# Performance work log

Measured on AMD Instinct MI355X. Metric: run time of the kernel, lower is better.

Reference implementation:

```python
import jax, jax.numpy as jnp
import numpy as np
from jax import lax

N_FFT = 2048
HOP = 512
N_ITER = 60
MOMENTUM = 0.99 / (1.0 + 0.99)  # torchaudio normalizes momentum/(1+momentum)
EPS = 1e-16
PAD = N_FFT // 2


def _hann(n):
    # periodic hann window, matches torch.hann_window(n)
    return 0.5 - 0.5 * jnp.cos(2.0 * jnp.pi * jnp.arange(n, dtype=jnp.float32) / n)


def _stft(x, window):
    # x: (B, L) real -> (B, F, T) complex. center=True, reflect pad, onesided, unnormalized.
    B, L = x.shape
    xp = jnp.pad(x, ((0, 0), (PAD, PAD)), mode='reflect')
    T = 1 + (L + 2 * PAD - N_FFT) // HOP
    idx = jnp.arange(T)[:, None] * HOP + jnp.arange(N_FFT)[None, :]  # (T, N)
    frames = xp[:, idx] * window  # (B, T, N)
    spec = jnp.fft.rfft(frames, axis=-1)  # (B, T, F)
    return jnp.swapaxes(spec, 1, 2)  # (B, F, T)


def _istft(spec, window):
    # spec: (B, F, T) complex -> (B, hop*(T-1)) real. Matches torch.istft(center=True).
    B, F, T = spec.shape
    frames = jnp.fft.irfft(jnp.swapaxes(spec, 1, 2), n=N_FFT, axis=-1) * window  # (B, T, N)
    L_pad = N_FFT + HOP * (T - 1)
    idx_flat = (jnp.arange(T)[:, None] * HOP + jnp.arange(N_FFT)[None, :]).reshape(-1)
    y = jnp.zeros((B, L_pad), frames.dtype).at[:, idx_flat].add(frames.reshape(B, -1))
    wsq = jnp.zeros((L_pad,), window.dtype).at[idx_flat].add(
        jnp.tile(window * window, T))
    y = y / jnp.where(wsq > 1e-11, wsq, 1.0)
    return y[:, PAD:L_pad - PAD]


def _griffin_lim(spec, window):
    # spec: (B, F, T) nonnegative magnitudes (power=1.0 so no pow needed)
    spec_c = spec.astype(jnp.complex64)
    angles0 = jnp.ones_like(spec_c)   # rand_init=False -> full of ones
    tprev0 = jnp.zeros_like(spec_c)

    def step(carry, _):
        angles, tprev = carry
        inv = _istft(spec_c * angles, window)
        rebuilt = _stft(inv, window)
        a = rebuilt - tprev * MOMENTUM
        a = a / (jnp.abs(a) + EPS)
        return (a, rebuilt), None

    (angles, _), _ = lax.scan(step, (angles0, tprev0), None, length=N_ITER)
    return _istft(spec_c * angles, window)


def setup_inputs() -> dict:
    key = jax.random.key(0)
    B, T, F = 4, 400, N_FFT // 2 + 1
    spectrogram = jax.random.uniform(key, (B, T, F), dtype=jnp.float32)
    return {"spectrogram": spectrogram}


def reference(spectrogram):
    window = _hann(N_FFT)
    spec = jnp.transpose(spectrogram, (0, 2, 1))  # (B, F, T)
    return _griffin_lim(spec, window)  # (B, HOP*(T-1))
```

## Files before the change

kernel.cpp:

```cpp
#include <hip/hip_runtime.h>
#include <math.h>

constexpr int BB   = 4;
constexpr int TT   = 400;
constexpr int FF   = 1025;
constexpr int NFFT = 2048;
constexpr int HOP  = 512;
constexpr int PADD = 1024;
constexpr int LL   = HOP * (TT - 1);
constexpr int LPAD = NFFT + HOP * (TT - 1);
constexpr int NITER = 60;
constexpr double MOM = 0.99 / 1.99;
constexpr double EPSV = 1e-16;
constexpr double DPI = 3.14159265358979323846;

constexpr size_t OFF_TW1024 = 0;
constexpr size_t OFF_TW2048 = 2048;
constexpr size_t OFF_TPR    = 4098;
constexpr size_t OFF_FRM    = 3284098;
constexpr size_t OFF_XP     = 6560898;
constexpr size_t OFF_WIN32  = 7386242;
constexpr size_t OFF_WSQ32  = 7387266;
constexpr size_t WS_DOUBLES = 7490434;

__device__ __forceinline__ double2 cmuld(double2 a, double2 b) {
    return make_double2(a.x * b.x - a.y * b.y, a.x * b.y + a.y * b.x);
}

__device__ __forceinline__ int swz(int f) { return f ^ ((f >> 4) & 7); }

__device__ __forceinline__ float np_cosf(float x) {
    const float rint_cvt = 0x1.800000p+23f;
    float qf = __builtin_fmaf(x, 0x1.45f306p-1f, rint_cvt) - rint_cvt;
    float r = __builtin_fmaf(qf, -0x1.921fb0p+0f, x);
    r = __builtin_fmaf(qf, -0x1.5110b4p-22f, r);
    r = __builtin_fmaf(qf, -0x1.846988p-48f, r);
    r = __builtin_fmaf(qf, -0x1.8cc966p-73f, r);
    int q = (int)qf + 1;
    float r2 = r * r;
    float cosp = __builtin_fmaf(0x1.98e616p-16f, r2, -0x1.6c06dcp-10f);
    cosp = __builtin_fmaf(cosp, r2, 0x1.55553cp-5f);
    cosp = __builtin_fmaf(cosp, r2, -0x1.000000p-1f);
    cosp = __builtin_fmaf(cosp, r2, 0x1.000000p+0f);
    float sinp = __builtin_fmaf(0x1.7d3bbcp-19f, r2, -0x1.a06bbap-13f);
    sinp = __builtin_fmaf(sinp, r2, 0x1.11119ap-7f);
    sinp = __builtin_fmaf(sinp, r2, -0x1.555548p-3f);
    sinp = sinp * r2;
    sinp = __builtin_fmaf(sinp, r, r);
    float res = (q & 1) ? cosp : sinp;
    return (q & 2) ? -res : res;
}

__global__ void k_init_tables(double2* tw1024, double2* tw2048, float* win) {
    int n = blockIdx.x * blockDim.x + threadIdx.x;
    if (n < 1024) {
        double th = -2.0 * DPI * (double)n / 1024.0;
        double s, c; sincos(th, &s, &c);
        tw1024[n] = make_double2(c, s);
    }
    if (n < 1025) {
        double th = -2.0 * DPI * (double)n / 2048.0;
        double s, c; sincos(th, &s, &c);
        tw2048[n] = make_double2(c, s);
    }
    if (n < 2048) {
        const float TWO_PI_F = 6.283185307179586f;
        float ang = __fdiv_rn(__fmul_rn(TWO_PI_F, (float)n), 2048.0f);
        float c = np_cosf(ang);
        win[n] = __fsub_rn(0.5f, __fmul_rn(0.5f, c));
    }
}

__global__ void k_init_wsq(const float* __restrict__ win, float* __restrict__ wsq) {
    int m = blockIdx.x * blockDim.x + threadIdx.x;
    if (m >= LPAD) return;
    int tlo = (m - (NFFT - HOP)) >> 9;
    if (tlo < 0) tlo = 0;
    int thi = m >> 9;
    if (thi > TT - 1) thi = TT - 1;
    float s = 0.0f;
    for (int t = tlo; t <= thi; ++t) {
        float w = win[m - (t << 9)];
        s = __fadd_rn(s, __fmul_rn(w, w));
    }
    wsq[m] = (s > 1e-11f) ? s : 1.0f;
}

__global__ void k_init_state(double2* __restrict__ tpr) {
    int i = blockIdx.x * blockDim.x + threadIdx.x;
    if (i < BB * TT * FF) tpr[i] = make_double2(0.0, 0.0);
}

template <int DIR, bool TW>
__device__ __forceinline__ void bfly4(double2 a, double2 b, double2 c, double2 d,
                                      double2 w1, double2 w2, double2 w3,
                                      double2& o0, double2& o1, double2& o2, double2& o3) {
    if (TW) {
        if (DIR > 0) { w1.y = -w1.y; w2.y = -w2.y; w3.y = -w3.y; }
        b = cmuld(b, w1);
        c = cmuld(c, w2);
        d = cmuld(d, w3);
    }
    double2 u0 = make_double2(a.x + c.x, a.y + c.y);
    double2 u1 = make_double2(a.x - c.x, a.y - c.y);
    double2 v0 = make_double2(b.x + d.x, b.y + d.y);
    double2 v1 = make_double2(b.x - d.x, b.y - d.y);
    o0 = make_double2(u0.x + v0.x, u0.y + v0.y);
    o2 = make_double2(u0.x - v0.x, u0.y - v0.y);
    if (DIR < 0) {
        o1 = make_double2(u1.x + v1.y, u1.y - v1.x);
        o3 = make_double2(u1.x - v1.y, u1.y + v1.x);
    } else {
        o1 = make_double2(u1.x - v1.y, u1.y + v1.x);
        o3 = make_double2(u1.x + v1.y, u1.y - v1.x);
    }
}

template <int DIR>
__device__ void fft1024_reg(double2 r[16], double2* S, const double2* __restrict__ tw, int tid) {
    const double2 wid = make_double2(1.0, 0.0);
    double2 e[4][4];
#pragma unroll
    for (int m = 0; m < 4; ++m)
        bfly4<DIR, false>(r[m], r[m + 4], r[m + 8], r[m + 12], wid, wid, wid,
                          e[m][0], e[m][1], e[m][2], e[m][3]);
    double2 g[4][4];
#pragma unroll
    for (int r1 = 0; r1 < 4; ++r1) {
        int t1 = r1 << 6;
        bfly4<DIR, true>(e[0][r1], e[1][r1], e[2][r1], e[3][r1],
                         tw[t1 & 1023], tw[(2 * t1) & 1023], tw[(3 * t1) & 1023],
                         g[r1][0], g[r1][1], g[r1][2], g[r1][3]);
    }
#pragma unroll
    for (int r1 = 0; r1 < 4; ++r1)
#pragma unroll
        for (int u = 0; u < 4; ++u)
            S[swz(16 * tid + r1 + 4 * u)] = g[r1][u];
    __syncthreads();
    double2 r2[16];
#pragma unroll
    for (int j = 0; j < 16; ++j) r2[j] = S[swz(tid + 64 * j)];
    const int kapp = tid & 15;
    const int aa = tid >> 4;
    double2 h[4][4];
    {
        int t = kapp << 4;
        double2 w1 = tw[t & 1023], w2 = tw[(2 * t) & 1023], w3 = tw[(3 * t) & 1023];
#pragma unroll
        for (int m = 0; m < 4; ++m)
            bfly4<DIR, true>(r2[m], r2[m + 4], r2[m + 8], r2[m + 12], w1, w2, w3,
                             h[m][0], h[m][1], h[m][2], h[m][3]);
    }
    double2 gg[4][4];
#pragma unroll
    for (int u = 0; u < 4; ++u) {
        int t = (kapp + 16 * u) << 2;
        bfly4<DIR, true>(h[0][u], h[1][u], h[2][u], h[3][u],
                         tw[t & 1023], tw[(2 * t) & 1023], tw[(3 * t) & 1023],
                         gg[u][0], gg[u][1], gg[u][2], gg[u][3]);
    }
#pragma unroll
    for (int u = 0; u < 4; ++u)
#pragma unroll
        for (int w = 0; w < 4; ++w)
            S[swz(256 * aa + kapp + 16 * u + 64 * w)] = gg[u][w];
    __syncthreads();
    double2 r4[16];
#pragma unroll
    for (int j = 0; j < 16; ++j) r4[j] = S[swz(tid + 64 * j)];
#pragma unroll
    for (int m = 0; m < 4; ++m) {
        int t = tid + 64 * m;
        bfly4<DIR, true>(r4[m], r4[m + 4], r4[m + 8], r4[m + 12],
                         tw[t & 1023], tw[(2 * t) & 1023], tw[(3 * t) & 1023],
                         r[m], r[m + 4], r[m + 8], r[m + 12]);
    }
}

__device__ __forceinline__ double2 phase_step(double2 zk, double2 zc, double2 w,
                                              double2 tp, float mgf, double2* Xk_out) {
    zc.y = -zc.y;
    double2 A = make_double2(0.5 * (zk.x + zc.x), 0.5 * (zk.y + zc.y));
    double2 D = make_double2(zk.x - zc.x, zk.y - zc.y);
    double2 Bv = make_double2(0.5 * D.y, -0.5 * D.x);
    double2 wB = cmuld(w, Bv);
    double2 Xk = make_double2(A.x + wB.x, A.y + wB.y);
    double2 a = make_double2(Xk.x - MOM * tp.x, Xk.y - MOM * tp.y);
    double r = sqrt(a.x * a.x + a.y * a.y);
    double d = r + EPSV;
    *Xk_out = Xk;
    double m = (double)mgf;
    return make_double2(m * (a.x / d), m * (a.y / d));
}

__device__ __forceinline__ double2 pretwist(double2 Xk, double2 Xc, double2 w) {
    Xc.y = -Xc.y;
    double2 A = make_double2(0.5 * (Xk.x + Xc.x), 0.5 * (Xk.y + Xc.y));
    double2 D = make_double2(0.5 * (Xk.x - Xc.x), 0.5 * (Xk.y - Xc.y));
    w.y = -w.y;
    double2 Bv = cmuld(w, D);
    return make_double2(A.x - Bv.y, A.y + Bv.x);
}

template <int DIR>
__device__ void fft1024_w(double2* buf, const double2* __restrict__ tw, int tid) {
#pragma unroll
    for (int s = 0; s < 5; ++s) {
        const int p = 1 << (2 * s);
        double2 o0[4], o1[4], o2[4], o3[4];
        int jj[4];
#pragma unroll
        for (int q = 0; q < 4; ++q) {
            int v = tid + 64 * q;
            int k = v & (p - 1);
            jj[q] = ((v - k) << 2) + k;
            int t1 = k << (8 - 2 * s);
            bfly4<DIR, true>(buf[v], buf[v + 256], buf[v + 512], buf[v + 768],
                             tw[t1 & 1023], tw[(2 * t1) & 1023], tw[(3 * t1) & 1023],
                             o0[q], o1[q], o2[q], o3[q]);
        }
        __syncthreads();
#pragma unroll
        for (int q = 0; q < 4; ++q) {
            buf[jj[q]]         = o0[q];
            buf[jj[q] + p]     = o1[q];
            buf[jj[q] + 2 * p] = o2[q];
            buf[jj[q] + 3 * p] = o3[q];
        }
        __syncthreads();
    }
}

__global__ __launch_bounds__(64) void k_istft_first(
    const float* __restrict__ mag,
    const double2* __restrict__ tw1024, const double2* __restrict__ tw2048,
    const float* __restrict__ win, double* __restrict__ frames_out) {
    __shared__ double2 S[1025];
    const int fid = blockIdx.x;
    const int tid = threadIdx.x;
    const float* mg = mag + (size_t)fid * FF;
#pragma unroll
    for (int q = 0; q < 8; ++q) {
        int k = tid + 64 * q;
        double mk = (double)mg[k];
        if (k == 0) {
            double m1024 = (double)mg[1024];
            double m512  = (double)mg[512];
            S[0]   = pretwist(make_double2(mk, 0.0),   make_double2(m1024, 0.0), tw2048[0]);
            S[512] = pretwist(make_double2(m512, 0.0), make_double2(m512, 0.0),  tw2048[512]);
        } else {
            int kp = 1024 - k;
            double mp = (double)mg[kp];
            S[k]  = pretwist(make_double2(mk, 0.0), make_double2(mp, 0.0), tw2048[k]);
            S[kp] = pretwist(make_double2(mp, 0.0), make_double2(mk, 0.0), tw2048[kp]);
        }
    }
    __syncthreads();
    fft1024_w<1>(S, tw1024, tid);
    double2* fr = reinterpret_cast<double2*>(frames_out + (size_t)fid * NFFT);
    const float2* w2 = reinterpret_cast<const float2*>(win);
#pragma unroll
    for (int q = 0; q < 16; ++q) {
        int m = tid + 64 * q;
        double2 z = S[m];
        float2 wv = w2[m];
        fr[m] = make_double2(z.x * (1.0 / 1024.0) * (double)wv.x,
                             z.y * (1.0 / 1024.0) * (double)wv.y);
    }
}

__global__ __launch_bounds__(256) void k_ola(
    const double* __restrict__ frames, const float* __restrict__ wsq,
    double* __restrict__ xp) {
    int bx = blockIdx.x;
    int bid = (bx & 7) * 403 + (bx >> 3);
    int gid = bid * 256 + threadIdx.x;
    int b = gid / LPAD;
    int p = gid - b * LPAD;
    int j = p - PADD;
    if (j < 0) j = -j;
    else if (j >= LL) j = 2 * LL - 2 - j;
    int m = j + PADD;
    int tlo = (m - (NFFT - HOP)) >> 9;
    if (tlo < 0) tlo = 0;
    int thi = m >> 9;
    if (thi > TT - 1) thi = TT - 1;
    const double* fb = frames + (size_t)b * TT * NFFT;
    double s = 0.0;
    for (int t = tlo; t <= thi; ++t) s += fb[(size_t)t * NFFT + (m - (t << 9))];
    xp[gid] = s / (double)wsq[m];
}

__global__ __launch_bounds__(64) void k_fused(
    const double* __restrict__ xp, double* __restrict__ frames_out,
    const float* __restrict__ mag, double2* __restrict__ tpr,
    const double2* __restrict__ tw1024, const double2* __restrict__ tw2048,
    const float* __restrict__ win) {
    __shared__ double2 S[1024];
    const int bx = blockIdx.x;
    const int fid = (bx & 7) * 200 + (bx >> 3);
    const int b = fid / TT;
    const int t = fid - b * TT;
    const int tid = threadIdx.x;
    const double2* xb = reinterpret_cast<const double2*>(xp + (size_t)b * LPAD + (size_t)t * HOP);
    const float2* w2 = reinterpret_cast<const float2*>(win);
    double2 r[16];
#pragma unroll
    for (int j = 0; j < 16; ++j) {
        int k = tid + 64 * j;
        double2 v = xb[k];
        float2 wv = w2[k];
        r[j] = make_double2(v.x * (double)wv.x, v.y * (double)wv.y);
    }
    fft1024_reg<-1>(r, S, tw1024, tid);
#pragma unroll
    for (int j = 0; j < 16; ++j) S[swz(tid + 64 * j)] = r[j];
    __syncthreads();
    size_t base = (size_t)fid * FF;
    const float* mg = mag + base;
#pragma unroll
    for (int q = 0; q < 8; ++q) {
        int k = tid + 64 * q;
        int kp = 1024 - k;
        double2 zk = S[swz(k)];
        double2 zc = S[swz(kp & 1023)];
        double2 wk = tw2048[k];
        double2 Xk;
        double2 Snew_k = phase_step(zk, zc, wk, tpr[base + k], mg[k], &Xk);
        tpr[base + k] = Xk;
        if (k == 0) {
            double2 X1024;
            double2 Snew_1024 = phase_step(zk, zk, tw2048[1024], tpr[base + 1024], mg[1024], &X1024);
            tpr[base + 1024] = X1024;
            double2 z512 = S[swz(512)];
            double2 X512;
            double2 Snew_512 = phase_step(z512, z512, tw2048[512], tpr[base + 512], mg[512], &X512);
            tpr[base + 512] = X512;
            double2 Xk0 = Snew_k;    Xk0.y = 0.0;
            double2 Xc0 = Snew_1024; Xc0.y = 0.0;
            S[swz(0)]   = pretwist(Xk0, Xc0, tw2048[0]);
            S[swz(512)] = pretwist(Snew_512, Snew_512, tw2048[512]);
        } else {
            double2 wp = tw2048[kp];
            double2 Xp;
            double2 Snew_p = phase_step(zc, zk, wp, tpr[base + kp], mg[kp], &Xp);
            tpr[base + kp] = Xp;
            S[swz(k)]  = pretwist(Snew_k, Snew_p, wk);
            S[swz(kp)] = pretwist(Snew_p, Snew_k, wp);
        }
    }
    __syncthreads();
#pragma unroll
    for (int j = 0; j < 16; ++j) r[j] = S[swz(tid + 64 * j)];
    fft1024_reg<1>(r, S, tw1024, tid);
    double2* fr = reinterpret_cast<double2*>(frames_out + (size_t)fid * NFFT);
#pragma unroll
    for (int j = 0; j < 16; ++j) {
        int m = tid + 64 * j;
        float2 wv = w2[m];
        fr[m] = make_double2(r[j].x * (1.0 / 1024.0) * (double)wv.x,
                             r[j].y * (1.0 / 1024.0) * (double)wv.y);
    }
}

__global__ __launch_bounds__(256) void k_ola_out(
    const double* __restrict__ frames, const float* __restrict__ wsq,
    float* __restrict__ out) {
    int bx = blockIdx.x;
    int bid = (bx & 7) * 399 + (bx >> 3);
    int gid = bid * 256 + threadIdx.x;
    int b = gid / LL;
    int j = gid - b * LL;
    int m = j + PADD;
    int tlo = (m - (NFFT - HOP)) >> 9;
    if (tlo < 0) tlo = 0;
    int thi = m >> 9;
    if (thi > TT - 1) thi = TT - 1;
    const double* fb = frames + (size_t)b * TT * NFFT;
    double s = 0.0;
    for (int t = tlo; t <= thi; ++t) s += fb[(size_t)t * NFFT + (m - (t << 9))];
    out[gid] = (float)(s / (double)wsq[m]);
}

extern "C" void kernel_launch(void* const* d_in, const int* in_sizes, int n_in,
                              void* d_out, int out_size, void* d_ws, size_t ws_size,
                              hipStream_t stream) {
    if (ws_size < WS_DOUBLES * sizeof(double)) return;
    const float* mag = (const float*)d_in[0];
    double* ws = (double*)d_ws;
    double2* tw1024 = (double2*)(ws + OFF_TW1024);
    double2* tw2048 = (double2*)(ws + OFF_TW2048);
    double2* tprv   = (double2*)(ws + OFF_TPR);
    double* frames  = ws + OFF_FRM;
    double* xp      = ws + OFF_XP;
    float* win      = (float*)(ws + OFF_WIN32);
    float* wsq      = (float*)(ws + OFF_WSQ32);

    k_init_tables<<<8, 256, 0, stream>>>(tw1024, tw2048, win);
    k_init_wsq<<<LPAD / 256, 256, 0, stream>>>(win, wsq);
    k_init_state<<<(BB * TT * FF + 255) / 256, 256, 0, stream>>>(tprv);

    k_istft_first<<<BB * TT, 64, 0, stream>>>(mag, tw1024, tw2048, win, frames);
    for (int it = 0; it < NITER; ++it) {
        k_ola<<<(BB * LPAD) / 256, 256, 0, stream>>>(frames, wsq, xp);
        k_fused<<<BB * TT, 64, 0, stream>>>(xp, frames, mag, tprv,
                                            tw1024, tw2048, win);
    }
    k_ola_out<<<(BB * LL) / 256, 256, 0, stream>>>(frames, wsq, (float*)d_out);
}
```

Measured before the change: 1.776 ms.

## Fuse overlap-add into per-frame STFT kernel with ping-pong frame buffers

Removes the separate overlap-add kernel and its intermediate padded signal buffer by having each frame block gather and normalize its overlapping frame contributions directly before the forward FFT. Frames are double-buffered so reads and writes within one launch do not race. This halves the launches per iteration and removes a global write/read pass, at the cost of redundant gathers (each sample recomputed by up to four frames) done by low-occupancy 64-thread blocks.

```diff
diff --git a/kernel.cpp b/kernel.cpp
--- a/kernel.cpp
+++ b/kernel.cpp
@@ -17,11 +17,11 @@
 constexpr size_t OFF_TW1024 = 0;
 constexpr size_t OFF_TW2048 = 2048;
 constexpr size_t OFF_TPR    = 4098;
-constexpr size_t OFF_FRM    = 3284098;
-constexpr size_t OFF_XP     = 6560898;
-constexpr size_t OFF_WIN32  = 7386242;
-constexpr size_t OFF_WSQ32  = 7387266;
-constexpr size_t WS_DOUBLES = 7490434;
+constexpr size_t OFF_FRM0   = 3284098;
+constexpr size_t OFF_FRM1   = 6560898;
+constexpr size_t OFF_WIN32  = 9837698;
+constexpr size_t OFF_WSQ32  = 9838722;
+constexpr size_t WS_DOUBLES = 9941890;
 
 __device__ __forceinline__ double2 cmuld(double2 a, double2 b) {
     return make_double2(a.x * b.x - a.y * b.y, a.x * b.y + a.y * b.x);
@@ -270,48 +270,43 @@
     }
 }
 
-__global__ __launch_bounds__(256) void k_ola(
-    const double* __restrict__ frames, const float* __restrict__ wsq,
-    double* __restrict__ xp) {
-    int bx = blockIdx.x;
-    int bid = (bx & 7) * 403 + (bx >> 3);
-    int gid = bid * 256 + threadIdx.x;
-    int b = gid / LPAD;
-    int p = gid - b * LPAD;
-    int j = p - PADD;
-    if (j < 0) j = -j;
-    else if (j >= LL) j = 2 * LL - 2 - j;
-    int m = j + PADD;
-    int tlo = (m - (NFFT - HOP)) >> 9;
-    if (tlo < 0) tlo = 0;
-    int thi = m >> 9;
-    if (thi > TT - 1) thi = TT - 1;
-    const double* fb = frames + (size_t)b * TT * NFFT;
-    double s = 0.0;
-    for (int t = tlo; t <= thi; ++t) s += fb[(size_t)t * NFFT + (m - (t << 9))];
-    xp[gid] = s / (double)wsq[m];
-}
-
-__global__ __launch_bounds__(64) void k_fused(
-    const double* __restrict__ xp, double* __restrict__ frames_out,
+__global__ __launch_bounds__(64) void k_mono(
+    const double* __restrict__ frames_in, double* __restrict__ frames_out,
     const float* __restrict__ mag, double2* __restrict__ tpr,
     const double2* __restrict__ tw1024, const double2* __restrict__ tw2048,
-    const float* __restrict__ win) {
+    const float* __restrict__ win, const float* __restrict__ wsq) {
     __shared__ double2 S[1024];
     const int bx = blockIdx.x;
     const int fid = (bx & 7) * 200 + (bx >> 3);
     const int b = fid / TT;
     const int t = fid - b * TT;
     const int tid = threadIdx.x;
-    const double2* xb = reinterpret_cast<const double2*>(xp + (size_t)b * LPAD + (size_t)t * HOP);
     const float2* w2 = reinterpret_cast<const float2*>(win);
+    const double* fb = frames_in + (size_t)b * TT * NFFT;
+    const int t512 = t * HOP;
     double2 r[16];
 #pragma unroll
     for (int j = 0; j < 16; ++j) {
         int k = tid + 64 * j;
-        double2 v = xb[k];
+        double xv0, xv1;
+#pragma unroll
+        for (int h = 0; h < 2; ++h) {
+            int p = t512 + 2 * k + h;
+            int jj = p - PADD;
+            if (jj < 0) jj = -jj;
+            else if (jj >= LL) jj = 2 * LL - 2 - jj;
+            int m = jj + PADD;
+            int tlo = (m - (NFFT - HOP)) >> 9;
+            if (tlo < 0) tlo = 0;
+            int thi = m >> 9;
+            if (thi > TT - 1) thi = TT - 1;
+            double s = 0.0;
+            for (int u = tlo; u <= thi; ++u) s += fb[(size_t)u * NFFT + (m - (u << 9))];
+            double val = s / (double)wsq[m];
+            if (h == 0) xv0 = val; else xv1 = val;
+        }
         float2 wv = w2[k];
-        r[j] = make_double2(v.x * (double)wv.x, v.y * (double)wv.y);
+        r[j] = make_double2(xv0 * (double)wv.x, xv1 * (double)wv.y);
     }
     fft1024_reg<-1>(r, S, tw1024, tid);
 #pragma unroll
@@ -392,8 +387,8 @@
     double2* tw1024 = (double2*)(ws + OFF_TW1024);
     double2* tw2048 = (double2*)(ws + OFF_TW2048);
     double2* tprv   = (double2*)(ws + OFF_TPR);
-    double* frames  = ws + OFF_FRM;
-    double* xp      = ws + OFF_XP;
+    double* frm0    = ws + OFF_FRM0;
+    double* frm1    = ws + OFF_FRM1;
     float* win      = (float*)(ws + OFF_WIN32);
     float* wsq      = (float*)(ws + OFF_WSQ32);
 
@@ -401,11 +396,12 @@
     k_init_wsq<<<LPAD / 256, 256, 0, stream>>>(win, wsq);
     k_init_state<<<(BB * TT * FF + 255) / 256, 256, 0, stream>>>(tprv);
 
-    k_istft_first<<<BB * TT, 64, 0, stream>>>(mag, tw1024, tw2048, win, frames);
+    k_istft_first<<<BB * TT, 64, 0, stream>>>(mag, tw1024, tw2048, win, frm0);
     for (int it = 0; it < NITER; ++it) {
-        k_ola<<<(BB * LPAD) / 256, 256, 0, stream>>>(frames, wsq, xp);
-        k_fused<<<BB * TT, 64, 0, stream>>>(xp, frames, mag, tprv,
-                                            tw1024, tw2048, win);
-    }
-    k_ola_out<<<(BB * LL) / 256, 256, 0, stream>>>(frames, wsq, (float*)d_out);
-}
+        double* fin  = (it & 1) ? frm1 : frm0;
+        double* fout = (it & 1) ? frm0 : frm1;
+        k_mono<<<BB * TT, 64, 0, stream>>>(fin, fout, mag, tprv,
+                                           tw1024, tw2048, win, wsq);
+    }
+    k_ola_out<<<(BB * LL) / 256, 256, 0, stream>>>(frm0, wsq, (float*)d_out);
+}
```

Result: slower. 3.047 ms (+71.5%).

## Process two frames per block in fused STFT kernel to share barriers

Applied to the files above, without the earlier changes.

The fused per-iteration kernel now handles two frames per 64-thread block. The two 1024-point FFTs are interleaved stage by stage, so each shared-memory barrier and the twiddle loads are shared between them and there is more independent work per thread. Stores to shared memory are also issued right after each butterfly. The launch uses half as many blocks. In exchange, registers and LDS per block double (two 16 KB buffers), which can lower occupancy and leaves only 800 blocks to spread across the CUs.

```diff
diff --git a/kernel.cpp b/kernel.cpp
--- a/kernel.cpp
+++ b/kernel.cpp
@@ -117,30 +117,29 @@
 }
 
 template <int DIR>
-__device__ void fft1024_reg(double2 r[16], double2* S, const double2* __restrict__ tw, int tid) {
+__device__ __forceinline__ void fft_stage01(double2 r[16], double2* S, const double2* __restrict__ tw, int tid) {
     const double2 wid = make_double2(1.0, 0.0);
     double2 e[4][4];
 #pragma unroll
     for (int m = 0; m < 4; ++m)
         bfly4<DIR, false>(r[m], r[m + 4], r[m + 8], r[m + 12], wid, wid, wid,
                           e[m][0], e[m][1], e[m][2], e[m][3]);
-    double2 g[4][4];
 #pragma unroll
     for (int r1 = 0; r1 < 4; ++r1) {
+        double2 g0, g1, g2, g3;
         int t1 = r1 << 6;
         bfly4<DIR, true>(e[0][r1], e[1][r1], e[2][r1], e[3][r1],
                          tw[t1 & 1023], tw[(2 * t1) & 1023], tw[(3 * t1) & 1023],
-                         g[r1][0], g[r1][1], g[r1][2], g[r1][3]);
-    }
-#pragma unroll
-    for (int r1 = 0; r1 < 4; ++r1)
-#pragma unroll
-        for (int u = 0; u < 4; ++u)
-            S[swz(16 * tid + r1 + 4 * u)] = g[r1][u];
-    __syncthreads();
-    double2 r2[16];
-#pragma unroll
-    for (int j = 0; j < 16; ++j) r2[j] = S[swz(tid + 64 * j)];
+                         g0, g1, g2, g3);
+        S[swz(16 * tid + r1)]      = g0;
+        S[swz(16 * tid + r1 + 4)]  = g1;
+        S[swz(16 * tid + r1 + 8)]  = g2;
+        S[swz(16 * tid + r1 + 12)] = g3;
+    }
+}
+
+template <int DIR>
+__device__ __forceinline__ void fft_stage23(double2 r2[16], double2* S, const double2* __restrict__ tw, int tid) {
     const int kapp = tid & 15;
     const int aa = tid >> 4;
     double2 h[4][4];
@@ -152,23 +151,22 @@
             bfly4<DIR, true>(r2[m], r2[m + 4], r2[m + 8], r2[m + 12], w1, w2, w3,
                              h[m][0], h[m][1], h[m][2], h[m][3]);
     }
-    double2 gg[4][4];
 #pragma unroll
     for (int u = 0; u < 4; ++u) {
+        double2 g0, g1, g2, g3;
         int t = (kapp + 16 * u) << 2;
         bfly4<DIR, true>(h[0][u], h[1][u], h[2][u], h[3][u],
                          tw[t & 1023], tw[(2 * t) & 1023], tw[(3 * t) & 1023],
-                         gg[u][0], gg[u][1], gg[u][2], gg[u][3]);
-    }
-#pragma unroll
-    for (int u = 0; u < 4; ++u)
-#pragma unroll
-        for (int w = 0; w < 4; ++w)
-            S[swz(256 * aa + kapp + 16 * u + 64 * w)] = gg[u][w];
-    __syncthreads();
-    double2 r4[16];
-#pragma unroll
-    for (int j = 0; j < 16; ++j) r4[j] = S[swz(tid + 64 * j)];
+                         g0, g1, g2, g3);
+        S[swz(256 * aa + kapp + 16 * u)]       = g0;
+        S[swz(256 * aa + kapp + 16 * u + 64)]  = g1;
+        S[swz(256 * aa + kapp + 16 * u + 128)] = g2;
+        S[swz(256 * aa + kapp + 16 * u + 192)] = g3;
+    }
+}
+
+template <int DIR>
+__device__ __forceinline__ void fft_stage4(double2 r4[16], double2 r[16], const double2* __restrict__ tw, int tid) {
 #pragma unroll
     for (int m = 0; m < 4; ++m) {
         int t = tid + 64 * m;
@@ -176,6 +174,29 @@
                          tw[t & 1023], tw[(2 * t) & 1023], tw[(3 * t) & 1023],
                          r[m], r[m + 4], r[m + 8], r[m + 12]);
     }
+}
+
+template <int DIR>
+__device__ void fft1024_reg2(double2 rA[16], double2 rB[16], double2* SA, double2* SBl,
+                             const double2* __restrict__ tw, int tid) {
+    fft_stage01<DIR>(rA, SA, tw, tid);
+    fft_stage01<DIR>(rB, SBl, tw, tid);
+    __syncthreads();
+    double2 r2A[16], r2B[16];
+#pragma unroll
+    for (int j = 0; j < 16; ++j) r2A[j] = SA[swz(tid + 64 * j)];
+#pragma unroll
+    for (int j = 0; j < 16; ++j) r2B[j] = SBl[swz(tid + 64 * j)];
+    fft_stage23<DIR>(r2A, SA, tw, tid);
+    fft_stage23<DIR>(r2B, SBl, tw, tid);
+    __syncthreads();
+    double2 r4A[16], r4B[16];
+#pragma unroll
+    for (int j = 0; j < 16; ++j) r4A[j] = SA[swz(tid + 64 * j)];
+#pragma unroll
+    for (int j = 0; j < 16; ++j) r4B[j] = SBl[swz(tid + 64 * j)];
+    fft_stage4<DIR>(r4A, rA, tw, tid);
+    fft_stage4<DIR>(r4B, rB, tw, tid);
 }
 
 __device__ __forceinline__ double2 phase_step(double2 zk, double2 zc, double2 w,
@@ -203,122 +224,9 @@
     return make_double2(A.x - Bv.y, A.y + Bv.x);
 }
 
-template <int DIR>
-__device__ void fft1024_w(double2* buf, const double2* __restrict__ tw, int tid) {
-#pragma unroll
-    for (int s = 0; s < 5; ++s) {
-        const int p = 1 << (2 * s);
-        double2 o0[4], o1[4], o2[4], o3[4];
-        int jj[4];
-#pragma unroll
-        for (int q = 0; q < 4; ++q) {
-            int v = tid + 64 * q;
-            int k = v & (p - 1);
-            jj[q] = ((v - k) << 2) + k;
-            int t1 = k << (8 - 2 * s);
-            bfly4<DIR, true>(buf[v], buf[v + 256], buf[v + 512], buf[v + 768],
-                             tw[t1 & 1023], tw[(2 * t1) & 1023], tw[(3 * t1) & 1023],
-                             o0[q], o1[q], o2[q], o3[q]);
-        }
-        __syncthreads();
-#pragma unroll
-        for (int q = 0; q < 4; ++q) {
-            buf[jj[q]]         = o0[q];
-            buf[jj[q] + p]     = o1[q];
-            buf[jj[q] + 2 * p] = o2[q];
-            buf[jj[q] + 3 * p] = o3[q];
-        }
-        __syncthreads();
-    }
-}
-
-__global__ __launch_bounds__(64) void k_istft_first(
-    const float* __restrict__ mag,
-    const double2* __restrict__ tw1024, const double2* __restrict__ tw2048,
-    const float* __restrict__ win, double* __restrict__ frames_out) {
-    __shared__ double2 S[1025];
-    const int fid = blockIdx.x;
-    const int tid = threadIdx.x;
-    const float* mg = mag + (size_t)fid * FF;
-#pragma unroll
-    for (int q = 0; q < 8; ++q) {
-        int k = tid + 64 * q;
-        double mk = (double)mg[k];
-        if (k == 0) {
-            double m1024 = (double)mg[1024];
-            double m512  = (double)mg[512];
-            S[0]   = pretwist(make_double2(mk, 0.0),   make_double2(m1024, 0.0), tw2048[0]);
-            S[512] = pretwist(make_double2(m512, 0.0), make_double2(m512, 0.0),  tw2048[512]);
-        } else {
-            int kp = 1024 - k;
-            double mp = (double)mg[kp];
-            S[k]  = pretwist(make_double2(mk, 0.0), make_double2(mp, 0.0), tw2048[k]);
-            S[kp] = pretwist(make_double2(mp, 0.0), make_double2(mk, 0.0), tw2048[kp]);
-        }
-    }
-    __syncthreads();
-    fft1024_w<1>(S, tw1024, tid);
-    double2* fr = reinterpret_cast<double2*>(frames_out + (size_t)fid * NFFT);
-    const float2* w2 = reinterpret_cast<const float2*>(win);
-#pragma unroll
-    for (int q = 0; q < 16; ++q) {
-        int m = tid + 64 * q;
-        double2 z = S[m];
-        float2 wv = w2[m];
-        fr[m] = make_double2(z.x * (1.0 / 1024.0) * (double)wv.x,
-                             z.y * (1.0 / 1024.0) * (double)wv.y);
-    }
-}
-
-__global__ __launch_bounds__(256) void k_ola(
-    const double* __restrict__ frames, const float* __restrict__ wsq,
-    double* __restrict__ xp) {
-    int bx = blockIdx.x;
-    int bid = (bx & 7) * 403 + (bx >> 3);
-    int gid = bid * 256 + threadIdx.x;
-    int b = gid / LPAD;
-    int p = gid - b * LPAD;
-    int j = p - PADD;
-    if (j < 0) j = -j;
-    else if (j >= LL) j = 2 * LL - 2 - j;
-    int m = j + PADD;
-    int tlo = (m - (NFFT - HOP)) >> 9;
-    if (tlo < 0) tlo = 0;
-    int thi = m >> 9;
-    if (thi > TT - 1) thi = TT - 1;
-    const double* fb = frames + (size_t)b * TT * NFFT;
-    double s = 0.0;
-    for (int t = tlo; t <= thi; ++t) s += fb[(size_t)t * NFFT + (m - (t << 9))];
-    xp[gid] = s / (double)wsq[m];
-}
-
-__global__ __launch_bounds__(64) void k_fused(
-    const double* __restrict__ xp, double* __restrict__ frames_out,
-    const float* __restrict__ mag, double2* __restrict__ tpr,
-    const double2* __restrict__ tw1024, const double2* __restrict__ tw2048,
-    const float* __restrict__ win) {
-    __shared__ double2 S[1024];
-    const int bx = blockIdx.x;
-    const int fid = (bx & 7) * 200 + (bx >> 3);
-    const int b = fid / TT;
-    const int t = fid - b * TT;
-    const int tid = threadIdx.x;
-    const double2* xb = reinterpret_cast<const double2*>(xp + (size_t)b * LPAD + (size_t)t * HOP);
-    const float2* w2 = reinterpret_cast<const float2*>(win);
-    double2 r[16];
-#pragma unroll
-    for (int j = 0; j < 16; ++j) {
-        int k = tid + 64 * j;
-        double2 v = xb[k];
-        float2 wv = w2[k];
-        r[j] = make_double2(v.x * (double)wv.x, v.y * (double)wv.y);
-    }
-    fft1024_reg<-1>(r, S, tw1024, tid);
-#pragma unroll
-    for (int j = 0; j < 16; ++j) S[swz(tid + 64 * j)] = r[j];
-    __syncthreads();
-    size_t base = (size_t)fid * FF;
-    const float* mg = mag + base;
+__device__ __forceinline__ void middle_phase(double2* S, double2* __restrict__ tpr,
+                                             size_t base, const float* __restrict__ mg,
+                                             const double2* __restrict__ tw2048, int tid) {
 #pragma unroll
     for (int q = 0; q < 8; ++q) {
         int k = tid + 64 * q;
@@ -350,17 +258,148 @@
             S[swz(kp)] = pretwist(Snew_p, Snew_k, wp);
         }
     }
+}
+
+template <int DIR>
+__device__ void fft1024_w(double2* buf, const double2* __restrict__ tw, int tid) {
+#pragma unroll
+    for (int s = 0; s < 5; ++s) {
+        const int p = 1 << (2 * s);
+        double2 o0[4], o1[4], o2[4], o3[4];
+        int jj[4];
+#pragma unroll
+        for (int q = 0; q < 4; ++q) {
+            int v = tid + 64 * q;
+            int k = v & (p - 1);
+            jj[q] = ((v - k) << 2) + k;
+            int t1 = k << (8 - 2 * s);
+            bfly4<DIR, true>(buf[v], buf[v + 256], buf[v + 512], buf[v + 768],
+                             tw[t1 & 1023], tw[(2 * t1) & 1023], tw[(3 * t1) & 1023],
+                             o0[q], o1[q], o2[q], o3[q]);
+        }
+        __syncthreads();
+#pragma unroll
+        for (int q = 0; q < 4; ++q) {
+            buf[jj[q]]         = o0[q];
+            buf[jj[q] + p]     = o1[q];
+            buf[jj[q] + 2 * p] = o2[q];
+            buf[jj[q] + 3 * p] = o3[q];
+        }
+        __syncthreads();
+    }
+}
+
+__global__ __launch_bounds__(64) void k_istft_first(
+    const float* __restrict__ mag,
+    const double2* __restrict__ tw1024, const double2* __restrict__ tw2048,
+    const float* __restrict__ win, double* __restrict__ frames_out) {
+    __shared__ double2 S[1025];
+    const int fid = blockIdx.x;
+    const int tid = threadIdx.x;
+    const float* mg = mag + (size_t)fid * FF;
+#pragma unroll
+    for (int q = 0; q < 8; ++q) {
+        int k = tid + 64 * q;
+        double mk = (double)mg[k];
+        if (k == 0) {
+            double m1024 = (double)mg[1024];
+            double m512  = (double)mg[512];
+            S[0]   = pretwist(make_double2(mk, 0.0),   make_double2(m1024, 0.0), tw2048[0]);
+            S[512] = pretwist(make_double2(m512, 0.0), make_double2(m512, 0.0),  tw2048[512]);
+        } else {
+            int kp = 1024 - k;
+            double mp = (double)mg[kp];
+            S[k]  = pretwist(make_double2(mk, 0.0), make_double2(mp, 0.0), tw2048[k]);
+            S[kp] = pretwist(make_double2(mp, 0.0), make_double2(mk, 0.0), tw2048[kp]);
+        }
+    }
     __syncthreads();
-#pragma unroll
-    for (int j = 0; j < 16; ++j) r[j] = S[swz(tid + 64 * j)];
-    fft1024_reg<1>(r, S, tw1024, tid);
+    fft1024_w<1>(S, tw1024, tid);
     double2* fr = reinterpret_cast<double2*>(frames_out + (size_t)fid * NFFT);
+    const float2* w2 = reinterpret_cast<const float2*>(win);
+#pragma unroll
+    for (int q = 0; q < 16; ++q) {
+        int m = tid + 64 * q;
+        double2 z = S[m];
+        float2 wv = w2[m];
+        fr[m] = make_double2(z.x * (1.0 / 1024.0) * (double)wv.x,
+                             z.y * (1.0 / 1024.0) * (double)wv.y);
+    }
+}
+
+__global__ __launch_bounds__(256) void k_ola(
+    const double* __restrict__ frames, const float* __restrict__ wsq,
+    double* __restrict__ xp) {
+    int bx = blockIdx.x;
+    int bid = (bx & 7) * 403 + (bx >> 3);
+    int gid = bid * 256 + threadIdx.x;
+    int b = gid / LPAD;
+    int p = gid - b * LPAD;
+    int j = p - PADD;
+    if (j < 0) j = -j;
+    else if (j >= LL) j = 2 * LL - 2 - j;
+    int m = j + PADD;
+    int tlo = (m - (NFFT - HOP)) >> 9;
+    if (tlo < 0) tlo = 0;
+    int thi = m >> 9;
+    if (thi > TT - 1) thi = TT - 1;
+    const double* fb = frames + (size_t)b * TT * NFFT;
+    double s = 0.0;
+    for (int t = tlo; t <= thi; ++t) s += fb[(size_t)t * NFFT + (m - (t << 9))];
+    xp[gid] = s / (double)wsq[m];
+}
+
+__global__ __launch_bounds__(64) void k_fused(
+    const double* __restrict__ xp, double* __restrict__ frames_out,
+    const float* __restrict__ mag, double2* __restrict__ tpr,
+    const double2* __restrict__ tw1024, const double2* __restrict__ tw2048,
+    const float* __restrict__ win) {
+    __shared__ double2 SA[1024];
+    __shared__ double2 SBl[1024];
+    const int bx = blockIdx.x;
+    const int s = (bx & 7) * 100 + (bx >> 3);
+    const int fid0 = 2 * s;
+    const int fid1 = 2 * s + 1;
+    const int b0 = fid0 / TT, t0 = fid0 - b0 * TT;
+    const int b1 = fid1 / TT, t1 = fid1 - b1 * TT;
+    const int tid = threadIdx.x;
+    const double2* xb0 = reinterpret_cast<const double2*>(xp + (size_t)b0 * LPAD + (size_t)t0 * HOP);
+    const double2* xb1 = reinterpret_cast<const double2*>(xp + (size_t)b1 * LPAD + (size_t)t1 * HOP);
+    const float2* w2 = reinterpret_cast<const float2*>(win);
+    double2 rA[16], rB[16];
+#pragma unroll
+    for (int j = 0; j < 16; ++j) {
+        int k = tid + 64 * j;
+        float2 wv = w2[k];
+        double2 v0 = xb0[k];
+        double2 v1 = xb1[k];
+        rA[j] = make_double2(v0.x * (double)wv.x, v0.y * (double)wv.y);
+        rB[j] = make_double2(v1.x * (double)wv.x, v1.y * (double)wv.y);
+    }
+    fft1024_reg2<-1>(rA, rB, SA, SBl, tw1024, tid);
+#pragma unroll
+    for (int j = 0; j < 16; ++j) SA[swz(tid + 64 * j)] = rA[j];
+#pragma unroll
+    for (int j = 0; j < 16; ++j) SBl[swz(tid + 64 * j)] = rB[j];
+    __syncthreads();
+    middle_phase(SA,  tpr, (size_t)fid0 * FF, mag + (size_t)fid0 * FF, tw2048, tid);
+    middle_phase(SBl, tpr, (size_t)fid1 * FF, mag + (size_t)fid1 * FF, tw2048, tid);
+    __syncthreads();
+#pragma unroll
+    for (int j = 0; j < 16; ++j) rA[j] = SA[swz(tid + 64 * j)];
+#pragma unroll
+    for (int j = 0; j < 16; ++j) rB[j] = SBl[swz(tid + 64 * j)];
+    fft1024_reg2<1>(rA, rB, SA, SBl, tw1024, tid);
+    double2* fr0 = reinterpret_cast<double2*>(frames_out + (size_t)fid0 * NFFT);
+    double2* fr1 = reinterpret_cast<double2*>(frames_out + (size_t)fid1 * NFFT);
 #pragma unroll
     for (int j = 0; j < 16; ++j) {
         int m = tid + 64 * j;
         float2 wv = w2[m];
-        fr[m] = make_double2(r[j].x * (1.0 / 1024.0) * (double)wv.x,
-                             r[j].y * (1.0 / 1024.0) * (double)wv.y);
+        fr0[m] = make_double2(rA[j].x * (1.0 / 1024.0) * (double)wv.x,
+                              rA[j].y * (1.0 / 1024.0) * (double)wv.y);
+        fr1[m] = make_double2(rB[j].x * (1.0 / 1024.0) * (double)wv.x,
+                              rB[j].y * (1.0 / 1024.0) * (double)wv.y);
     }
 }
 
@@ -404,8 +443,8 @@
     k_istft_first<<<BB * TT, 64, 0, stream>>>(mag, tw1024, tw2048, win, frames);
     for (int it = 0; it < NITER; ++it) {
         k_ola<<<(BB * LPAD) / 256, 256, 0, stream>>>(frames, wsq, xp);
-        k_fused<<<BB * TT, 64, 0, stream>>>(xp, frames, mag, tprv,
-                                            tw1024, tw2048, win);
+        k_fused<<<BB * TT / 2, 64, 0, stream>>>(xp, frames, mag, tprv,
+                                                tw1024, tw2048, win);
     }
     k_ola_out<<<(BB * LL) / 256, 256, 0, stream>>>(frames, wsq, (float*)d_out);
 }
```

Measured after the change: 2.129 ms. +19.9%, slower.

## Recompute previous-iteration STFT instead of storing tprev state in global memory

Applied to the files above, without the earlier changes.

Removes the per-bin tprev buffer (read and write of complex doubles every iteration). Instead, the previous iteration's time-domain signal is kept in a ping-pong xp buffer and re-transformed with a second FFT inside the fused kernel to recover the previous rebuilt spectrum. This trades global-memory traffic for a doubled forward-FFT workload and twice the shared memory per block, which may reduce occupancy.

```diff
diff --git a/kernel.cpp b/kernel.cpp
--- a/kernel.cpp
+++ b/kernel.cpp
@@ -16,12 +16,12 @@
 
 constexpr size_t OFF_TW1024 = 0;
 constexpr size_t OFF_TW2048 = 2048;
-constexpr size_t OFF_TPR    = 4098;
-constexpr size_t OFF_FRM    = 3284098;
-constexpr size_t OFF_XP     = 6560898;
-constexpr size_t OFF_WIN32  = 7386242;
-constexpr size_t OFF_WSQ32  = 7387266;
-constexpr size_t WS_DOUBLES = 7490434;
+constexpr size_t OFF_FRM    = 4098;
+constexpr size_t OFF_XP0    = 3280898;
+constexpr size_t OFF_XP1    = 4106242;
+constexpr size_t OFF_WIN32  = 4931586;
+constexpr size_t OFF_WSQ32  = 4932610;
+constexpr size_t WS_DOUBLES = 5035778;
 
 __device__ __forceinline__ double2 cmuld(double2 a, double2 b) {
     return make_double2(a.x * b.x - a.y * b.y, a.x * b.y + a.y * b.x);
@@ -86,11 +86,6 @@
     wsq[m] = (s > 1e-11f) ? s : 1.0f;
 }
 
-__global__ void k_init_state(double2* __restrict__ tpr) {
-    int i = blockIdx.x * blockDim.x + threadIdx.x;
-    if (i < BB * TT * FF) tpr[i] = make_double2(0.0, 0.0);
-}
-
 template <int DIR, bool TW>
 __device__ __forceinline__ void bfly4(double2 a, double2 b, double2 c, double2 d,
                                       double2 w1, double2 w2, double2 w3,
@@ -178,18 +173,19 @@
     }
 }
 
-__device__ __forceinline__ double2 phase_step(double2 zk, double2 zc, double2 w,
-                                              double2 tp, float mgf, double2* Xk_out) {
+__device__ __forceinline__ double2 untw(double2 zk, double2 zc, double2 w) {
     zc.y = -zc.y;
     double2 A = make_double2(0.5 * (zk.x + zc.x), 0.5 * (zk.y + zc.y));
     double2 D = make_double2(zk.x - zc.x, zk.y - zc.y);
     double2 Bv = make_double2(0.5 * D.y, -0.5 * D.x);
     double2 wB = cmuld(w, Bv);
-    double2 Xk = make_double2(A.x + wB.x, A.y + wB.y);
+    return make_double2(A.x + wB.x, A.y + wB.y);
+}
+
+__device__ __forceinline__ double2 mom_phase(double2 Xk, double2 tp, float mgf) {
     double2 a = make_double2(Xk.x - MOM * tp.x, Xk.y - MOM * tp.y);
     double r = sqrt(a.x * a.x + a.y * a.y);
     double d = r + EPSV;
-    *Xk_out = Xk;
     double m = (double)mgf;
     return make_double2(m * (a.x / d), m * (a.y / d));
 }
@@ -293,32 +289,49 @@
 }
 
 __global__ __launch_bounds__(64) void k_fused(
-    const double* __restrict__ xp, double* __restrict__ frames_out,
-    const float* __restrict__ mag, double2* __restrict__ tpr,
+    const double* __restrict__ xp_cur, const double* __restrict__ xp_prev,
+    double* __restrict__ frames_out, const float* __restrict__ mag,
     const double2* __restrict__ tw1024, const double2* __restrict__ tw2048,
-    const float* __restrict__ win) {
+    const float* __restrict__ win, int first) {
     __shared__ double2 S[1024];
+    __shared__ double2 SP[1024];
     const int bx = blockIdx.x;
     const int fid = (bx & 7) * 200 + (bx >> 3);
     const int b = fid / TT;
     const int t = fid - b * TT;
     const int tid = threadIdx.x;
-    const double2* xb = reinterpret_cast<const double2*>(xp + (size_t)b * LPAD + (size_t)t * HOP);
     const float2* w2 = reinterpret_cast<const float2*>(win);
+    const size_t xoff = (size_t)b * LPAD + (size_t)t * HOP;
     double2 r[16];
-#pragma unroll
-    for (int j = 0; j < 16; ++j) {
-        int k = tid + 64 * j;
-        double2 v = xb[k];
-        float2 wv = w2[k];
-        r[j] = make_double2(v.x * (double)wv.x, v.y * (double)wv.y);
+    if (!first) {
+        const double2* xbp = reinterpret_cast<const double2*>(xp_prev + xoff);
+#pragma unroll
+        for (int j = 0; j < 16; ++j) {
+            int k = tid + 64 * j;
+            double2 v = xbp[k];
+            float2 wv = w2[k];
+            r[j] = make_double2(v.x * (double)wv.x, v.y * (double)wv.y);
+        }
+        fft1024_reg<-1>(r, SP, tw1024, tid);
+#pragma unroll
+        for (int j = 0; j < 16; ++j) SP[swz(tid + 64 * j)] = r[j];
+    }
+    {
+        const double2* xbc = reinterpret_cast<const double2*>(xp_cur + xoff);
+#pragma unroll
+        for (int j = 0; j < 16; ++j) {
+            int k = tid + 64 * j;
+            double2 v = xbc[k];
+            float2 wv = w2[k];
+            r[j] = make_double2(v.x * (double)wv.x, v.y * (double)wv.y);
+        }
     }
     fft1024_reg<-1>(r, S, tw1024, tid);
 #pragma unroll
     for (int j = 0; j < 16; ++j) S[swz(tid + 64 * j)] = r[j];
     __syncthreads();
-    size_t base = (size_t)fid * FF;
-    const float* mg = mag + base;
+    const float* mg = mag + (size_t)fid * FF;
+    const double2 zero2 = make_double2(0.0, 0.0);
 #pragma unroll
     for (int q = 0; q < 8; ++q) {
         int k = tid + 64 * q;
@@ -326,26 +339,37 @@
         double2 zk = S[swz(k)];
         double2 zc = S[swz(kp & 1023)];
         double2 wk = tw2048[k];
-        double2 Xk;
-        double2 Snew_k = phase_step(zk, zc, wk, tpr[base + k], mg[k], &Xk);
-        tpr[base + k] = Xk;
+        double2 Xk = untw(zk, zc, wk);
+        double2 XkP = zero2, XpP = zero2;
+        double2 zkP, zcP;
+        if (!first) {
+            zkP = SP[swz(k)];
+            zcP = SP[swz(kp & 1023)];
+            XkP = untw(zkP, zcP, wk);
+        }
+        double2 Snew_k = mom_phase(Xk, XkP, mg[k]);
         if (k == 0) {
-            double2 X1024;
-            double2 Snew_1024 = phase_step(zk, zk, tw2048[1024], tpr[base + 1024], mg[1024], &X1024);
-            tpr[base + 1024] = X1024;
+            double2 X1024 = untw(zk, zk, tw2048[1024]);
+            double2 X1024P = zero2;
             double2 z512 = S[swz(512)];
-            double2 X512;
-            double2 Snew_512 = phase_step(z512, z512, tw2048[512], tpr[base + 512], mg[512], &X512);
-            tpr[base + 512] = X512;
+            double2 X512 = untw(z512, z512, tw2048[512]);
+            double2 X512P = zero2;
+            if (!first) {
+                X1024P = untw(zkP, zkP, tw2048[1024]);
+                double2 z512P = SP[swz(512)];
+                X512P = untw(z512P, z512P, tw2048[512]);
+            }
+            double2 Snew_1024 = mom_phase(X1024, X1024P, mg[1024]);
+            double2 Snew_512  = mom_phase(X512,  X512P,  mg[512]);
             double2 Xk0 = Snew_k;    Xk0.y = 0.0;
             double2 Xc0 = Snew_1024; Xc0.y = 0.0;
             S[swz(0)]   = pretwist(Xk0, Xc0, tw2048[0]);
             S[swz(512)] = pretwist(Snew_512, Snew_512, tw2048[512]);
         } else {
             double2 wp = tw2048[kp];
-            double2 Xp;
-            double2 Snew_p = phase_step(zc, zk, wp, tpr[base + kp], mg[kp], &Xp);
-            tpr[base + kp] = Xp;
+            double2 Xp = untw(zc, zk, wp);
+            if (!first) XpP = untw(zcP, zkP, wp);
+            double2 Snew_p = mom_phase(Xp, XpP, mg[kp]);
             S[swz(k)]  = pretwist(Snew_k, Snew_p, wk);
             S[swz(kp)] = pretwist(Snew_p, Snew_k, wp);
         }
@@ -391,21 +415,22 @@
     double* ws = (double*)d_ws;
     double2* tw1024 = (double2*)(ws + OFF_TW1024);
     double2* tw2048 = (double2*)(ws + OFF_TW2048);
-    double2* tprv   = (double2*)(ws + OFF_TPR);
     double* frames  = ws + OFF_FRM;
-    double* xp      = ws + OFF_XP;
+    double* xp0     = ws + OFF_XP0;
+    double* xp1     = ws + OFF_XP1;
     float* win      = (float*)(ws + OFF_WIN32);
     float* wsq      = (float*)(ws + OFF_WSQ32);
 
     k_init_tables<<<8, 256, 0, stream>>>(tw1024, tw2048, win);
     k_init_wsq<<<LPAD / 256, 256, 0, stream>>>(win, wsq);
-    k_init_state<<<(BB * TT * FF + 255) / 256, 256, 0, stream>>>(tprv);
 
     k_istft_first<<<BB * TT, 64, 0, stream>>>(mag, tw1024, tw2048, win, frames);
     for (int it = 0; it < NITER; ++it) {
-        k_ola<<<(BB * LPAD) / 256, 256, 0, stream>>>(frames, wsq, xp);
-        k_fused<<<BB * TT, 64, 0, stream>>>(xp, frames, mag, tprv,
-                                            tw1024, tw2048, win);
+        double* cur  = (it & 1) ? xp1 : xp0;
+        double* prev = (it & 1) ? xp0 : xp1;
+        k_ola<<<(BB * LPAD) / 256, 256, 0, stream>>>(frames, wsq, cur);
+        k_fused<<<BB * TT, 64, 0, stream>>>(cur, prev, frames, mag,
+                                            tw1024, tw2048, win, it == 0 ? 1 : 0);
     }
     k_ola_out<<<(BB * LL) / 256, 256, 0, stream>>>(frames, wsq, (float*)d_out);
 }
```

New measurement: 2.921 ms. 1.64x slower.
